# Kernel optimization log

Hardware: AMD Instinct MI355X
Metric: run time of the kernel (lower is better)

The kernel has to match this reference:

```python
import jax, jax.numpy as jnp
import numpy as np

B, N = 32, 32768
IN_F, HID, N_HIDDEN, OUT_F = 2, 128, 3, 3
OMEGA0 = 30.0

# (W_shape, b_shape, apply_sine) per layer, matching SIREN.get_param_shapes(rank=None)
LAYER_SPECS = (
    [((HID, IN_F), (HID,), True)]
    + [((HID, HID), (HID,), True) for _ in range(N_HIDDEN)]
    + [((OUT_F, HID), (OUT_F,), False)]
)
TOTAL_PARAMS = sum(int(np.prod(W)) + int(np.prod(b)) for W, b, _ in LAYER_SPECS)  # 50307


def setup_inputs() -> dict:
    key = jax.random.key(0)
    k1, k2 = jax.random.split(key)
    x_coords_batch = jax.random.uniform(k1, (B, N, IN_F), dtype=jnp.float32) * 2.0 - 1.0
    # small-scale params, as SIREN init produces values in roughly +-sqrt(6/fan_in)/omega_0
    flat_params_batch = jax.random.normal(k2, (B, TOTAL_PARAMS), dtype=jnp.float32) * 0.02
    return {"x_coords_batch": x_coords_batch, "flat_params_batch": flat_params_batch}


def reference(x_coords_batch, flat_params_batch):
    x = x_coords_batch  # [B, N, d_in]
    b = x.shape[0]
    idx = 0
    for (out_f, in_f), b_shape, apply_sine in LAYER_SPECS:
        nW = out_f * in_f
        W = flat_params_batch[:, idx:idx + nW].reshape(b, out_f, in_f)
        idx += nW
        # bmm(x, W^T): [B,N,in] x [B,in,out] -> [B,N,out]
        x = jnp.einsum('bni,boi->bno', x, W)
        nb = b_shape[0]
        bias = flat_params_batch[:, idx:idx + nb].reshape(b, 1, nb)
        idx += nb
        x = x + bias
        if apply_sine:
            x = jnp.sin(OMEGA0 * x)
    return x
```

## Files before the change

kernel.cpp:

```cpp
#include <hip/hip_runtime.h>
#include <stdint.h>


typedef _Float16 f16x8 __attribute__((ext_vector_type(8)));
typedef __fp16 h16x2 __attribute__((ext_vector_type(2)));
typedef float f32x4 __attribute__((ext_vector_type(4)));

#define MFMA16 __builtin_amdgcn_mfma_f32_16x16x32_f16

#define B_ 32
#define N_ 32768
#define NTHR 1024
#define NWAVE 16
#define OMEGA_SC 4.77464829275686f

#define OFF_W1 0
#define OFF_B1 256
#define OFF_W2 384
#define OFF_B2 16768
#define OFF_W3 16896
#define OFF_B3 33280
#define OFF_W4 33408
#define OFF_B4 49792
#define OFF_W5 49920
#define OFF_B5 50304
#define NPARAM 50307

#define WO_L2H 0
#define WO_W2L 32768
#define WO_L3H 65536
#define WO_L4H 98304
#define WO_L5H 131072
#define WO_W1X 135168
#define WO_W1Y 135680
#define WO_B1S 136192
#define LDS_BIAS 136704
#define LDSSET 138240

__device__ __forceinline__ float sin_rev(float t) {
    return __builtin_amdgcn_sinf(t);
}

__device__ __forceinline__ uint32_t pack2(_Float16 a, _Float16 b) {
    union { _Float16 h[2]; uint32_t u; } x;
    x.h[0] = a; x.h[1] = b;
    return x.u;
}

__device__ __forceinline__ void sin_split_pk(float a0, float a1,
                                             uint32_t& hw, uint32_t& lw) {
    float s0 = sin_rev(a0), s1 = sin_rev(a1);
    union { h16x2 v; uint32_t u; } x, y;
    x.v = __builtin_amdgcn_cvt_pkrtz(s0, s1);
    float l0 = s0 - (float)x.v[0], l1 = s1 - (float)x.v[1];
    y.v = __builtin_amdgcn_cvt_pkrtz(l0, l1);
    hw = x.u; lw = y.u;
}

__global__ __launch_bounds__(NTHR, 4)
void siren_main(const float* __restrict__ xg,
                const float* __restrict__ pg,
                float* __restrict__ out) {
    extern __shared__ __align__(16) char smem[];

    const int t = threadIdx.x;
    const int b = blockIdx.x;
    const int grp = blockIdx.y;
    const float* p = pg + (size_t)b * NPARAM;

    for (int it = t; it < 6528; it += NTHR) {
        const int u = it >> 6, l = it & 63;
        if (u < 100) {
            int li, c, mt;
            if (u < 96) { li = u >> 5; int r = u & 31; c = r >> 3; mt = r & 7; }
            else        { li = 3; c = u - 96; mt = 0; }
            const int m = l & 15, gA = l >> 4;
            int wOff; size_t dstH; bool lo = false;
            if (li == 0)      { wOff = OFF_W2; dstH = WO_L2H; lo = true; }
            else if (li == 1) { wOff = OFF_W3; dstH = WO_L3H; }
            else if (li == 2) { wOff = OFF_W4; dstH = WO_L4H; }
            else              { wOff = OFF_W5; dstH = WO_L5H; }
            const int j = (li == 3) ? m : (16 * mt + m);
            const int f0 = 16 * c + 4 * gA;
            const float sc = (li == 3) ? 1.0f : OMEGA_SC;

            float v[8];
            if (li == 3 && m >= 3) {
#pragma unroll
                for (int e = 0; e < 8; ++e) v[e] = 0.f;
            } else {
                float4 a  = *(const float4*)(p + wOff + j * 128 + f0);
                float4 bq = *(const float4*)(p + wOff + j * 128 + f0 + 64);
                v[0] = sc * a.x;  v[1] = sc * a.y;  v[2] = sc * a.z;  v[3] = sc * a.w;
                v[4] = sc * bq.x; v[5] = sc * bq.y; v[6] = sc * bq.z; v[7] = sc * bq.w;
            }
            f16x8 hv, lv;
#pragma unroll
            for (int e = 0; e < 8; ++e) {
                _Float16 hh = (_Float16)v[e];
                hv[e] = hh;
                lv[e] = (_Float16)(v[e] - (float)hh);
            }
            size_t idx = (li == 3) ? (size_t)(c * 64 + l) * 16
                                   : (size_t)((c * 8 + mt) * 64 + l) * 16;
            *(f16x8*)(smem + dstH + idx) = hv;
            if (lo) *(f16x8*)(smem + WO_W2L + idx) = lv;
        } else {
            int s = ((u - 100) << 6) + l;
            int c = s >> 5, k = s & 31, gq = k >> 3, e = k & 7;
            int f = 16 * c + ((e & 4) ? 64 : 0) + 4 * gq + (e & 3);
            ((float*)(smem + WO_W1X))[s] = OMEGA_SC * p[OFF_W1 + 2 * f];
            ((float*)(smem + WO_W1Y))[s] = OMEGA_SC * p[OFF_W1 + 2 * f + 1];
            ((float*)(smem + WO_B1S))[s] = OMEGA_SC * p[OFF_B1 + f];
        }
    }
    float* sB = (float*)(smem + LDS_BIAS);
    if (t < 384) {
        int li = t >> 7, f = t & 127;
        sB[t] = OMEGA_SC * p[(li == 0 ? OFF_B2 : li == 1 ? OFF_B3 : OFF_B4) + f];
    }
    const float b5_0 = p[OFF_B5], b5_1 = p[OFF_B5 + 1], b5_2 = p[OFF_B5 + 2];
    __syncthreads();

    const int lane = t & 63;
    const int wv = t >> 6;
    const int n = lane & 15;
    const int g = lane >> 4;
    const int lb = lane * 16;

    const char* L2Hp = smem + WO_L2H;
    const char* W2Lp = smem + WO_W2L;
    const char* L3Hp = smem + WO_L3H;
    const char* L4Hp = smem + WO_L4H;
    const char* L5Hp = smem + WO_L5H;
    const float* W1X = (const float*)(smem + WO_W1X);
    const float* W1Y = (const float*)(smem + WO_W1Y);
    const float* B1S = (const float*)(smem + WO_B1S);

    union UF { f16x8 v; uint32_t w[4]; };

    auto initb2 = [&](f32x4 (&A)[2][8], int li) {
#pragma unroll
        for (int mt = 0; mt < 8; ++mt) {
            f32x4 bb = *(const f32x4*)&sB[li * 128 + 16 * mt + 4 * g];
            A[0][mt] = bb;
            A[1][mt] = bb;
        }
    };

    auto epi_hi2 = [&](const f32x4 (&A)[2][8], UF (&Xh)[2][4]) {
#pragma unroll
        for (int pp = 0; pp < 2; ++pp)
#pragma unroll
            for (int c = 0; c < 4; ++c) {
                _Float16 hh[8];
#pragma unroll
                for (int r = 0; r < 4; ++r) {
                    hh[r]     = (_Float16)sin_rev(A[pp][c][r]);
                    hh[4 + r] = (_Float16)sin_rev(A[pp][c + 4][r]);
                }
                Xh[pp][c].w[0] = pack2(hh[0], hh[1]); Xh[pp][c].w[1] = pack2(hh[2], hh[3]);
                Xh[pp][c].w[2] = pack2(hh[4], hh[5]); Xh[pp][c].w[3] = pack2(hh[6], hh[7]);
            }
    };

#pragma unroll 1
    for (int tile = wv; tile < 128; tile += NWAVE) {
        const int ptb = grp * 4096 + tile * 32;
        const float2 xy0 = ((const float2*)xg)[(size_t)b * N_ + ptb + n];
        const float2 xy1 = ((const float2*)xg)[(size_t)b * N_ + ptb + 16 + n];

        f32x4 A2[2][8];
        initb2(A2, 0);
#pragma unroll
        for (int c = 0; c < 4; ++c) {
            UF X1h[2], X1l[2];
            {
                const int s0 = c * 32 + g * 8;
                float4 wxa = *(const float4*)(W1X + s0), wxb = *(const float4*)(W1X + s0 + 4);
                float4 wya = *(const float4*)(W1Y + s0), wyb = *(const float4*)(W1Y + s0 + 4);
                float4 bba = *(const float4*)(B1S + s0), bbb = *(const float4*)(B1S + s0 + 4);
                float wx[8] = {wxa.x, wxa.y, wxa.z, wxa.w, wxb.x, wxb.y, wxb.z, wxb.w};
                float wy[8] = {wya.x, wya.y, wya.z, wya.w, wyb.x, wyb.y, wyb.z, wyb.w};
                float bc[8] = {bba.x, bba.y, bba.z, bba.w, bbb.x, bbb.y, bbb.z, bbb.w};
#pragma unroll
                for (int pp = 0; pp < 2; ++pp) {
                    const float px = pp ? xy1.x : xy0.x;
                    const float py = pp ? xy1.y : xy0.y;
                    float a[8];
#pragma unroll
                    for (int e = 0; e < 8; ++e)
                        a[e] = fmaf(px, wx[e], fmaf(py, wy[e], bc[e]));
                    sin_split_pk(a[0], a[1], X1h[pp].w[0], X1l[pp].w[0]);
                    sin_split_pk(a[2], a[3], X1h[pp].w[1], X1l[pp].w[1]);
                    sin_split_pk(a[4], a[5], X1h[pp].w[2], X1l[pp].w[2]);
                    sin_split_pk(a[6], a[7], X1h[pp].w[3], X1l[pp].w[3]);
                }
            }
            __builtin_amdgcn_s_setprio(1);
#pragma unroll
            for (int mt = 0; mt < 8; ++mt) {
                f16x8 ah = *(const f16x8*)(L2Hp + (c * 8 + mt) * 1024 + lb);
                f16x8 al = *(const f16x8*)(W2Lp + (c * 8 + mt) * 1024 + lb);
#pragma unroll
                for (int pp = 0; pp < 2; ++pp) {
                    A2[pp][mt] = MFMA16(ah, X1h[pp].v, A2[pp][mt], 0, 0, 0);
                    A2[pp][mt] = MFMA16(ah, X1l[pp].v, A2[pp][mt], 0, 0, 0);
                    A2[pp][mt] = MFMA16(al, X1h[pp].v, A2[pp][mt], 0, 0, 0);
                }
            }
            __builtin_amdgcn_s_setprio(0);
        }

        UF X2h[2][4];
        epi_hi2(A2, X2h);

        f32x4 A3[2][8];
        initb2(A3, 1);
        __builtin_amdgcn_s_setprio(1);
#pragma unroll
        for (int c = 0; c < 4; ++c)
#pragma unroll
            for (int mt = 0; mt < 8; ++mt) {
                f16x8 ah = *(const f16x8*)(L3Hp + (c * 8 + mt) * 1024 + lb);
#pragma unroll
                for (int pp = 0; pp < 2; ++pp)
                    A3[pp][mt] = MFMA16(ah, X2h[pp][c].v, A3[pp][mt], 0, 0, 0);
            }
        __builtin_amdgcn_s_setprio(0);

        UF X3h[2][4];
        epi_hi2(A3, X3h);

        f32x4 A4[2][8];
        initb2(A4, 2);
        __builtin_amdgcn_s_setprio(1);
#pragma unroll
        for (int c = 0; c < 4; ++c)
#pragma unroll
            for (int mt = 0; mt < 8; ++mt) {
                f16x8 ah = *(const f16x8*)(L4Hp + (c * 8 + mt) * 1024 + lb);
#pragma unroll
                for (int pp = 0; pp < 2; ++pp)
                    A4[pp][mt] = MFMA16(ah, X3h[pp][c].v, A4[pp][mt], 0, 0, 0);
            }
        __builtin_amdgcn_s_setprio(0);

        UF X4h[2][4];
        epi_hi2(A4, X4h);

        f32x4 a5[2] = {{0.f, 0.f, 0.f, 0.f}, {0.f, 0.f, 0.f, 0.f}};
        __builtin_amdgcn_s_setprio(1);
#pragma unroll
        for (int c = 0; c < 4; ++c) {
            f16x8 ah = *(const f16x8*)(L5Hp + c * 1024 + lb);
#pragma unroll
            for (int pp = 0; pp < 2; ++pp)
                a5[pp] = MFMA16(ah, X4h[pp][c].v, a5[pp], 0, 0, 0);
        }
        __builtin_amdgcn_s_setprio(0);

        if (g == 0) {
#pragma unroll
            for (int pp = 0; pp < 2; ++pp) {
                size_t o = ((size_t)b * N_ + ptb + pp * 16 + n) * 3;
                out[o]     = a5[pp][0] + b5_0;
                out[o + 1] = a5[pp][1] + b5_1;
                out[o + 2] = a5[pp][2] + b5_2;
            }
        }
    }
}

extern "C" void kernel_launch(void* const* d_in, const int* in_sizes, int n_in,
                              void* d_out, int out_size, void* d_ws, size_t ws_size,
                              hipStream_t stream) {
    (void)in_sizes; (void)n_in; (void)out_size; (void)d_ws; (void)ws_size;
    const float* x = (const float*)d_in[0];
    const float* p = (const float*)d_in[1];
    float* o = (float*)d_out;

    static bool attr_done = false;
    if (!attr_done) {
        (void)hipFuncSetAttribute(reinterpret_cast<const void*>(siren_main),
                                  hipFuncAttributeMaxDynamicSharedMemorySize, LDSSET);
        attr_done = true;
    }
    siren_main<<<dim3(32, 8), NTHR, LDSSET, stream>>>(x, p, o);
}
```

Before: 205.6 us.

## Switch to 32x32x16 MFMA tiles and compute first layer on MFMA

Replaces the 16x16x32 MFMA tiling (two 16-point sub-tiles per wave) with 32x32x16 MFMA over 32 points per wave, and re-lays out all LDS weight fragments to match. The first layer's coordinate-linear map is now done with an MFMA using split-fp16 hi/lo weights and inputs plus a bias column, instead of per-lane scalar FMAs. The aim is fewer MFMA issues and fewer LDS fragment loads per point, and less VALU work in layer 1. In exchange it needs 16-wide accumulators and more registers, and the fp16-split first layer may lose a little precision.

```diff
diff --git a/kernel.cpp b/kernel.cpp
--- a/kernel.cpp
+++ b/kernel.cpp
@@ -5,8 +5,9 @@
 typedef _Float16 f16x8 __attribute__((ext_vector_type(8)));
 typedef __fp16 h16x2 __attribute__((ext_vector_type(2)));
 typedef float f32x4 __attribute__((ext_vector_type(4)));
-
-#define MFMA16 __builtin_amdgcn_mfma_f32_16x16x32_f16
+typedef float f32x16 __attribute__((ext_vector_type(16)));
+
+#define MFMA32(a, b, c) __builtin_amdgcn_mfma_f32_32x32x16_f16((a), (b), (c), 0, 0, 0)
 
 #define B_ 32
 #define N_ 32768
@@ -31,11 +32,9 @@
 #define WO_L3H 65536
 #define WO_L4H 98304
 #define WO_L5H 131072
-#define WO_W1X 135168
-#define WO_W1Y 135680
-#define WO_B1S 136192
-#define LDS_BIAS 136704
-#define LDSSET 138240
+#define WO_W1E 139264
+#define WO_BIA 143360
+#define LDSSET 144896
 
 __device__ __forceinline__ float sin_rev(float t) {
     return __builtin_amdgcn_sinf(t);
@@ -44,6 +43,12 @@
 __device__ __forceinline__ uint32_t pack2(_Float16 a, _Float16 b) {
     union { _Float16 h[2]; uint32_t u; } x;
     x.h[0] = a; x.h[1] = b;
+    return x.u;
+}
+
+__device__ __forceinline__ uint32_t pkrtz_u32(float a, float b) {
+    union { h16x2 v; uint32_t u; } x;
+    x.v = __builtin_amdgcn_cvt_pkrtz(a, b);
     return x.u;
 }
 
@@ -68,29 +73,30 @@
     const int grp = blockIdx.y;
     const float* p = pg + (size_t)b * NPARAM;
 
-    for (int it = t; it < 6528; it += NTHR) {
+    for (int it = t; it < 114 * 64; it += NTHR) {
         const int u = it >> 6, l = it & 63;
-        if (u < 100) {
-            int li, c, mt;
-            if (u < 96) { li = u >> 5; int r = u & 31; c = r >> 3; mt = r & 7; }
-            else        { li = 3; c = u - 96; mt = 0; }
-            const int m = l & 15, gA = l >> 4;
+        if (u < 104) {
+            int li, ks, mtA;
+            if (u < 96) { li = u >> 5; int r = u & 31; ks = r >> 2; mtA = r & 3; }
+            else        { li = 3; ks = u - 96; mtA = 0; }
+            const int mrow = l & 31, hi = l >> 5;
+            const int q = ks >> 1, s = ks & 1;
+            const int f0 = 32 * q + 16 * s + 4 * hi;
             int wOff; size_t dstH; bool lo = false;
             if (li == 0)      { wOff = OFF_W2; dstH = WO_L2H; lo = true; }
             else if (li == 1) { wOff = OFF_W3; dstH = WO_L3H; }
             else if (li == 2) { wOff = OFF_W4; dstH = WO_L4H; }
             else              { wOff = OFF_W5; dstH = WO_L5H; }
-            const int j = (li == 3) ? m : (16 * mt + m);
-            const int f0 = 16 * c + 4 * gA;
+            const int j = 32 * mtA + mrow;
             const float sc = (li == 3) ? 1.0f : OMEGA_SC;
 
             float v[8];
-            if (li == 3 && m >= 3) {
+            if (li == 3 && mrow >= 3) {
 #pragma unroll
                 for (int e = 0; e < 8; ++e) v[e] = 0.f;
             } else {
                 float4 a  = *(const float4*)(p + wOff + j * 128 + f0);
-                float4 bq = *(const float4*)(p + wOff + j * 128 + f0 + 64);
+                float4 bq = *(const float4*)(p + wOff + j * 128 + f0 + 8);
                 v[0] = sc * a.x;  v[1] = sc * a.y;  v[2] = sc * a.z;  v[3] = sc * a.w;
                 v[4] = sc * bq.x; v[5] = sc * bq.y; v[6] = sc * bq.z; v[7] = sc * bq.w;
             }
@@ -101,31 +107,44 @@
                 hv[e] = hh;
                 lv[e] = (_Float16)(v[e] - (float)hh);
             }
-            size_t idx = (li == 3) ? (size_t)(c * 64 + l) * 16
-                                   : (size_t)((c * 8 + mt) * 64 + l) * 16;
+            size_t idx = (li == 3) ? (size_t)(ks * 64 + l) * 16
+                                   : (size_t)((ks * 4 + mtA) * 64 + l) * 16;
             *(f16x8*)(smem + dstH + idx) = hv;
             if (lo) *(f16x8*)(smem + WO_W2L + idx) = lv;
+        } else if (u < 108) {
+            const int mtA = u - 104;
+            const int mrow = l & 31, hi = l >> 5;
+            const int j = 32 * mtA + mrow;
+            float wx = OMEGA_SC * p[OFF_W1 + 2 * j];
+            float wy = OMEGA_SC * p[OFF_W1 + 2 * j + 1];
+            float b1 = OMEGA_SC * p[OFF_B1 + j];
+            _Float16 wxh = (_Float16)wx, wyh = (_Float16)wy, b1h = (_Float16)b1;
+            _Float16 wxl = (_Float16)(wx - (float)wxh);
+            _Float16 wyl = (_Float16)(wy - (float)wyh);
+            _Float16 b1l = (_Float16)(b1 - (float)b1h);
+            f16x8 hv;
+            if (hi == 0) {
+                hv[0] = wxh; hv[1] = wxh; hv[2] = wxl; hv[3] = wyh;
+                hv[4] = wyh; hv[5] = wyl; hv[6] = b1h; hv[7] = b1l;
+            } else {
+#pragma unroll
+                for (int e = 0; e < 8; ++e) hv[e] = (_Float16)0.f;
+            }
+            *(f16x8*)(smem + WO_W1E + (size_t)(mtA * 64 + l) * 16) = hv;
         } else {
-            int s = ((u - 100) << 6) + l;
-            int c = s >> 5, k = s & 31, gq = k >> 3, e = k & 7;
-            int f = 16 * c + ((e & 4) ? 64 : 0) + 4 * gq + (e & 3);
-            ((float*)(smem + WO_W1X))[s] = OMEGA_SC * p[OFF_W1 + 2 * f];
-            ((float*)(smem + WO_W1Y))[s] = OMEGA_SC * p[OFF_W1 + 2 * f + 1];
-            ((float*)(smem + WO_B1S))[s] = OMEGA_SC * p[OFF_B1 + f];
-        }
-    }
-    float* sB = (float*)(smem + LDS_BIAS);
-    if (t < 384) {
-        int li = t >> 7, f = t & 127;
-        sB[t] = OMEGA_SC * p[(li == 0 ? OFF_B2 : li == 1 ? OFF_B3 : OFF_B4) + f];
+            int s2 = ((u - 108) << 6) + l;
+            int li = s2 >> 7, f = s2 & 127;
+            ((float*)(smem + WO_BIA))[s2] =
+                OMEGA_SC * p[(li == 0 ? OFF_B2 : li == 1 ? OFF_B3 : OFF_B4) + f];
+        }
     }
     const float b5_0 = p[OFF_B5], b5_1 = p[OFF_B5 + 1], b5_2 = p[OFF_B5 + 2];
     __syncthreads();
 
     const int lane = t & 63;
     const int wv = t >> 6;
-    const int n = lane & 15;
-    const int g = lane >> 4;
+    const int n = lane & 31;
+    const int hi = lane >> 5;
     const int lb = lane * 16;
 
     const char* L2Hp = smem + WO_L2H;
@@ -133,141 +152,130 @@
     const char* L3Hp = smem + WO_L3H;
     const char* L4Hp = smem + WO_L4H;
     const char* L5Hp = smem + WO_L5H;
-    const float* W1X = (const float*)(smem + WO_W1X);
-    const float* W1Y = (const float*)(smem + WO_W1Y);
-    const float* B1S = (const float*)(smem + WO_B1S);
+    const char* W1Ep = smem + WO_W1E;
+    const float* sBf = (const float*)(smem + WO_BIA);
 
     union UF { f16x8 v; uint32_t w[4]; };
 
-    auto initb2 = [&](f32x4 (&A)[2][8], int li) {
-#pragma unroll
-        for (int mt = 0; mt < 8; ++mt) {
-            f32x4 bb = *(const f32x4*)&sB[li * 128 + 16 * mt + 4 * g];
-            A[0][mt] = bb;
-            A[1][mt] = bb;
-        }
+    auto initb = [&](f32x16 (&A)[4], int li) {
+#pragma unroll
+        for (int mtA = 0; mtA < 4; ++mtA)
+#pragma unroll
+            for (int bb = 0; bb < 4; ++bb) {
+                f32x4 tv = *(const f32x4*)(sBf + li * 128 + 32 * mtA + 8 * bb + 4 * hi);
+                A[mtA][4 * bb + 0] = tv[0]; A[mtA][4 * bb + 1] = tv[1];
+                A[mtA][4 * bb + 2] = tv[2]; A[mtA][4 * bb + 3] = tv[3];
+            }
     };
 
-    auto epi_hi2 = [&](const f32x4 (&A)[2][8], UF (&Xh)[2][4]) {
-#pragma unroll
-        for (int pp = 0; pp < 2; ++pp)
-#pragma unroll
-            for (int c = 0; c < 4; ++c) {
-                _Float16 hh[8];
-#pragma unroll
-                for (int r = 0; r < 4; ++r) {
-                    hh[r]     = (_Float16)sin_rev(A[pp][c][r]);
-                    hh[4 + r] = (_Float16)sin_rev(A[pp][c + 4][r]);
-                }
-                Xh[pp][c].w[0] = pack2(hh[0], hh[1]); Xh[pp][c].w[1] = pack2(hh[2], hh[3]);
-                Xh[pp][c].w[2] = pack2(hh[4], hh[5]); Xh[pp][c].w[3] = pack2(hh[6], hh[7]);
+    auto epi_hi = [&](const f32x16 (&A)[4], UF (&Xh)[8]) {
+#pragma unroll
+        for (int q = 0; q < 4; ++q)
+#pragma unroll
+            for (int s = 0; s < 2; ++s) {
+                float sv[8];
+#pragma unroll
+                for (int j = 0; j < 8; ++j) sv[j] = sin_rev(A[q][8 * s + j]);
+                UF& X = Xh[2 * q + s];
+                X.w[0] = pkrtz_u32(sv[0], sv[1]);
+                X.w[1] = pkrtz_u32(sv[2], sv[3]);
+                X.w[2] = pkrtz_u32(sv[4], sv[5]);
+                X.w[3] = pkrtz_u32(sv[6], sv[7]);
             }
     };
 
 #pragma unroll 1
     for (int tile = wv; tile < 128; tile += NWAVE) {
         const int ptb = grp * 4096 + tile * 32;
-        const float2 xy0 = ((const float2*)xg)[(size_t)b * N_ + ptb + n];
-        const float2 xy1 = ((const float2*)xg)[(size_t)b * N_ + ptb + 16 + n];
-
-        f32x4 A2[2][8];
-        initb2(A2, 0);
-#pragma unroll
-        for (int c = 0; c < 4; ++c) {
-            UF X1h[2], X1l[2];
-            {
-                const int s0 = c * 32 + g * 8;
-                float4 wxa = *(const float4*)(W1X + s0), wxb = *(const float4*)(W1X + s0 + 4);
-                float4 wya = *(const float4*)(W1Y + s0), wyb = *(const float4*)(W1Y + s0 + 4);
-                float4 bba = *(const float4*)(B1S + s0), bbb = *(const float4*)(B1S + s0 + 4);
-                float wx[8] = {wxa.x, wxa.y, wxa.z, wxa.w, wxb.x, wxb.y, wxb.z, wxb.w};
-                float wy[8] = {wya.x, wya.y, wya.z, wya.w, wyb.x, wyb.y, wyb.z, wyb.w};
-                float bc[8] = {bba.x, bba.y, bba.z, bba.w, bbb.x, bbb.y, bbb.z, bbb.w};
-#pragma unroll
-                for (int pp = 0; pp < 2; ++pp) {
-                    const float px = pp ? xy1.x : xy0.x;
-                    const float py = pp ? xy1.y : xy0.y;
-                    float a[8];
-#pragma unroll
-                    for (int e = 0; e < 8; ++e)
-                        a[e] = fmaf(px, wx[e], fmaf(py, wy[e], bc[e]));
-                    sin_split_pk(a[0], a[1], X1h[pp].w[0], X1l[pp].w[0]);
-                    sin_split_pk(a[2], a[3], X1h[pp].w[1], X1l[pp].w[1]);
-                    sin_split_pk(a[4], a[5], X1h[pp].w[2], X1l[pp].w[2]);
-                    sin_split_pk(a[6], a[7], X1h[pp].w[3], X1l[pp].w[3]);
+        const float2 xy = ((const float2*)xg)[(size_t)b * N_ + ptb + n];
+
+        UF B1;
+        {
+            _Float16 xh = (_Float16)xy.x, yh = (_Float16)xy.y;
+            _Float16 xl = (_Float16)(xy.x - (float)xh);
+            _Float16 yl = (_Float16)(xy.y - (float)yh);
+            B1.w[0] = (hi == 0) ? pack2(xh, xl) : 0u;
+            B1.w[1] = (hi == 0) ? pack2(xh, yh) : 0u;
+            B1.w[2] = (hi == 0) ? pack2(yl, yh) : 0u;
+            B1.w[3] = (hi == 0) ? 0x3C003C00u : 0u;
+        }
+
+        f32x16 A2[4];
+        initb(A2, 0);
+#pragma unroll
+        for (int q = 0; q < 4; ++q) {
+            f16x8 a1 = *(const f16x8*)(W1Ep + (size_t)(q * 64 + lane) * 16);
+            f32x16 c1;
+#pragma unroll
+            for (int i = 0; i < 16; ++i) c1[i] = 0.f;
+            c1 = MFMA32(a1, B1.v, c1);
+#pragma unroll
+            for (int s = 0; s < 2; ++s) {
+                UF X1h, X1l;
+                sin_split_pk(c1[8 * s + 0], c1[8 * s + 1], X1h.w[0], X1l.w[0]);
+                sin_split_pk(c1[8 * s + 2], c1[8 * s + 3], X1h.w[1], X1l.w[1]);
+                sin_split_pk(c1[8 * s + 4], c1[8 * s + 5], X1h.w[2], X1l.w[2]);
+                sin_split_pk(c1[8 * s + 6], c1[8 * s + 7], X1h.w[3], X1l.w[3]);
+                const int ks = 2 * q + s;
+                __builtin_amdgcn_s_setprio(1);
+#pragma unroll
+                for (int mtA = 0; mtA < 4; ++mtA) {
+                    f16x8 ah = *(const f16x8*)(L2Hp + (size_t)((ks * 4 + mtA) * 64) * 16 + lb);
+                    f16x8 al = *(const f16x8*)(W2Lp + (size_t)((ks * 4 + mtA) * 64) * 16 + lb);
+                    A2[mtA] = MFMA32(ah, X1h.v, A2[mtA]);
+                    A2[mtA] = MFMA32(ah, X1l.v, A2[mtA]);
+                    A2[mtA] = MFMA32(al, X1h.v, A2[mtA]);
                 }
-            }
-            __builtin_amdgcn_s_setprio(1);
-#pragma unroll
-            for (int mt = 0; mt < 8; ++mt) {
-                f16x8 ah = *(const f16x8*)(L2Hp + (c * 8 + mt) * 1024 + lb);
-                f16x8 al = *(const f16x8*)(W2Lp + (c * 8 + mt) * 1024 + lb);
-#pragma unroll
-                for (int pp = 0; pp < 2; ++pp) {
-                    A2[pp][mt] = MFMA16(ah, X1h[pp].v, A2[pp][mt], 0, 0, 0);
-                    A2[pp][mt] = MFMA16(ah, X1l[pp].v, A2[pp][mt], 0, 0, 0);
-                    A2[pp][mt] = MFMA16(al, X1h[pp].v, A2[pp][mt], 0, 0, 0);
-                }
-            }
-            __builtin_amdgcn_s_setprio(0);
-        }
-
-        UF X2h[2][4];
-        epi_hi2(A2, X2h);
-
-        f32x4 A3[2][8];
-        initb2(A3, 1);
+                __builtin_amdgcn_s_setprio(0);
+            }
+        }
+
+        UF X2h[8];
+        epi_hi(A2, X2h);
+        f32x16 A3[4];
+        initb(A3, 1);
         __builtin_amdgcn_s_setprio(1);
 #pragma unroll
-        for (int c = 0; c < 4; ++c)
-#pragma unroll
-            for (int mt = 0; mt < 8; ++mt) {
-                f16x8 ah = *(const f16x8*)(L3Hp + (c * 8 + mt) * 1024 + lb);
-#pragma unroll
-                for (int pp = 0; pp < 2; ++pp)
-                    A3[pp][mt] = MFMA16(ah, X2h[pp][c].v, A3[pp][mt], 0, 0, 0);
+        for (int ks = 0; ks < 8; ++ks)
+#pragma unroll
+            for (int mtA = 0; mtA < 4; ++mtA) {
+                f16x8 ah = *(const f16x8*)(L3Hp + (size_t)((ks * 4 + mtA) * 64) * 16 + lb);
+                A3[mtA] = MFMA32(ah, X2h[ks].v, A3[mtA]);
             }
         __builtin_amdgcn_s_setprio(0);
 
-        UF X3h[2][4];
-        epi_hi2(A3, X3h);
-
-        f32x4 A4[2][8];
-        initb2(A4, 2);
+        UF X3h[8];
+        epi_hi(A3, X3h);
+        f32x16 A4[4];
+        initb(A4, 2);
         __builtin_amdgcn_s_setprio(1);
 #pragma unroll
-        for (int c = 0; c < 4; ++c)
-#pragma unroll
-            for (int mt = 0; mt < 8; ++mt) {
-                f16x8 ah = *(const f16x8*)(L4Hp + (c * 8 + mt) * 1024 + lb);
-#pragma unroll
-                for (int pp = 0; pp < 2; ++pp)
-                    A4[pp][mt] = MFMA16(ah, X3h[pp][c].v, A4[pp][mt], 0, 0, 0);
+        for (int ks = 0; ks < 8; ++ks)
+#pragma unroll
+            for (int mtA = 0; mtA < 4; ++mtA) {
+                f16x8 ah = *(const f16x8*)(L4Hp + (size_t)((ks * 4 + mtA) * 64) * 16 + lb);
+                A4[mtA] = MFMA32(ah, X3h[ks].v, A4[mtA]);
             }
         __builtin_amdgcn_s_setprio(0);
 
-        UF X4h[2][4];
-        epi_hi2(A4, X4h);
-
-        f32x4 a5[2] = {{0.f, 0.f, 0.f, 0.f}, {0.f, 0.f, 0.f, 0.f}};
+        UF X4h[8];
+        epi_hi(A4, X4h);
+        f32x16 a5;
+#pragma unroll
+        for (int i = 0; i < 16; ++i) a5[i] = 0.f;
         __builtin_amdgcn_s_setprio(1);
 #pragma unroll
-        for (int c = 0; c < 4; ++c) {
-            f16x8 ah = *(const f16x8*)(L5Hp + c * 1024 + lb);
-#pragma unroll
-            for (int pp = 0; pp < 2; ++pp)
-                a5[pp] = MFMA16(ah, X4h[pp][c].v, a5[pp], 0, 0, 0);
+        for (int ks = 0; ks < 8; ++ks) {
+            f16x8 ah = *(const f16x8*)(L5Hp + (size_t)(ks * 64) * 16 + lb);
+            a5 = MFMA32(ah, X4h[ks].v, a5);
         }
         __builtin_amdgcn_s_setprio(0);
 
-        if (g == 0) {
-#pragma unroll
-            for (int pp = 0; pp < 2; ++pp) {
-                size_t o = ((size_t)b * N_ + ptb + pp * 16 + n) * 3;
-                out[o]     = a5[pp][0] + b5_0;
-                out[o + 1] = a5[pp][1] + b5_1;
-                out[o + 2] = a5[pp][2] + b5_2;
-            }
+        if (hi == 0) {
+            size_t o = ((size_t)b * N_ + ptb + n) * 3;
+            out[o]     = a5[0] + b5_0;
+            out[o + 1] = a5[1] + b5_1;
+            out[o + 2] = a5[2] + b5_2;
         }
     }
 }
```

Measured after the change: 233.0 us. +13.4%, slower.
